# Performance work log

Measured on AMD Instinct MI355X. Metric: run time of the kernel, lower is better.

The kernel has to match this reference:

```python
import jax, jax.numpy as jnp
import numpy as np

IMG_SIZE = 224  # matches init_kwargs img_size


def setup_inputs() -> dict:
    key = jax.random.key(0)
    k1, k2, k3 = jax.random.split(key, 3)
    B, N = 128, 16384
    points = jax.random.uniform(k1, (B, N, 3), dtype=jnp.float32, minval=-1.0, maxval=1.0)
    azimuth = jax.random.uniform(k2, (B,), dtype=jnp.float32, minval=0.0, maxval=2.0 * np.pi)
    elevation = jax.random.uniform(k3, (B,), dtype=jnp.float32, minval=-0.5, maxval=0.5)
    return {"points": points, "azimuth": azimuth, "elevation": elevation}


def _rotation_matrices(azimuth, elevation):
    cა, sა = jnp.cos(azimuth), jnp.sin(azimuth)
    ce, se = jnp.cos(elevation), jnp.sin(elevation)
    z = jnp.zeros_like(cა)
    o = jnp.ones_like(cა)
    # R_az: rotation about y-axis, shape (B,3,3)
    R_az = jnp.stack([
        jnp.stack([cა, z, sა], -1),
        jnp.stack([z, o, z], -1),
        jnp.stack([-sა, z, cა], -1),
    ], axis=-2)
    # R_el: rotation about x-axis
    R_el = jnp.stack([
        jnp.stack([o, z, z], -1),
        jnp.stack([z, ce, -se], -1),
        jnp.stack([z, se, ce], -1),
    ], axis=-2)
    return jnp.einsum('bij,bjk->bik', R_el, R_az)


def reference(points, azimuth, elevation):
    B, N, _ = points.shape
    H = W = IMG_SIZE
    R = _rotation_matrices(azimuth, elevation)                 # (B,3,3)
    rotated = jnp.einsum('bni,bji->bnj', points, R)            # points @ R^T -> (B,N,3)

    points_2d = rotated[..., :2]
    z = rotated[..., 2]
    z_min = jnp.min(z, axis=1, keepdims=True)
    z_max = jnp.max(z, axis=1, keepdims=True)
    feat = 0.3 + 0.7 * (z - z_min) / (z_max - z_min + 1e-6)    # (B,N)

    px = (points_2d[..., 0] + 1.0) * 0.5 * W - 0.5
    py = (points_2d[..., 1] + 1.0) * 0.5 * H - 0.5
    px1 = jnp.floor(px); py1 = jnp.floor(py)
    px2 = px1 + 1.0;     py2 = py1 + 1.0

    w11 = (px2 - px) * (py2 - py)
    w12 = (px2 - px) * (py - py1)
    w21 = (px - px1) * (py2 - py)
    w22 = (px - px1) * (py - py1)

    mask = (px1 >= 0) & (py1 >= 0) & (px2 < W) & (py2 < H)     # (B,N)
    # fuse mask + feature into the weights instead of compacting (jit-friendly)
    vals = jnp.stack([w11, w12, w21, w22], axis=-1)            # (B,N,4)
    vals = vals * (feat * mask.astype(feat.dtype))[..., None]

    px1i = jnp.clip(px1, 0, W - 1).astype(jnp.int32)
    py1i = jnp.clip(py1, 0, H - 1).astype(jnp.int32)
    px2i = jnp.clip(px2, 0, W - 1).astype(jnp.int32)
    py2i = jnp.clip(py2, 0, H - 1).astype(jnp.int32)
    base = (jnp.arange(B, dtype=jnp.int32) * (H * W))[:, None]  # (B,1)
    idx = jnp.stack([
        base + py1i * W + px1i,
        base + py2i * W + px1i,
        base + py1i * W + px2i,
        base + py2i * W + px2i,
    ], axis=-1)                                                 # (B,N,4)

    image = jnp.zeros(B * H * W, dtype=vals.dtype)
    image = image.at[idx.reshape(-1)].add(vals.reshape(-1))
    image = image.reshape(B, 1, H, W)
    return jnp.broadcast_to(image, (B, 3, H, W))
```

## Files before the change

kernel.cpp:

```cpp
#include <hip/hip_runtime.h>

#define IMG 224
#define HW (IMG * IMG)
#define NB 128
#define NPTS 16384

#define QUARTERS 4
#define RPB (IMG / QUARTERS)
#define TILE_FLOATS (RPB * IMG)

#define PARAMS_STRIDE 12

__global__ __launch_bounds__(1024) void k_minmax(const float* __restrict__ pts,
                                                 const float* __restrict__ az,
                                                 const float* __restrict__ el,
                                                 float* __restrict__ params) {
    const int b = blockIdx.x;
    const int tid = threadIdx.x;

    float sa, ca, se, ce;
    __sincosf(az[b], &sa, &ca);
    __sincosf(el[b], &se, &ce);
    const float r20 = -ce * sa, r21 = se, r22 = ce * ca;

    const float* __restrict__ pb = pts + (size_t)b * NPTS * 3;

    float zmin = 1e30f, zmax = -1e30f;
    for (int n = tid; n < NPTS; n += 1024) {
        const float x = pb[n * 3 + 0];
        const float y = pb[n * 3 + 1];
        const float z = pb[n * 3 + 2];
        const float rz = r20 * x + r21 * y + r22 * z;
        zmin = fminf(zmin, rz);
        zmax = fmaxf(zmax, rz);
    }

    __shared__ float smin[1024], smax[1024];
    smin[tid] = zmin;
    smax[tid] = zmax;
    __syncthreads();
    for (int s = 512; s > 0; s >>= 1) {
        if (tid < s) {
            smin[tid] = fminf(smin[tid], smin[tid + s]);
            smax[tid] = fmaxf(smax[tid], smax[tid + s]);
        }
        __syncthreads();
    }

    if (tid == 0) {
        float* P = params + (size_t)b * PARAMS_STRIDE;
        P[0] = ca;       P[1] = 0.f; P[2] = sa;
        P[3] = se * sa;  P[4] = ce;  P[5] = -se * ca;
        P[6] = r20;      P[7] = r21; P[8] = r22;
        P[9] = smin[0];
        P[10] = 0.7f / (smax[0] - smin[0] + 1e-6f);
    }
}

__global__ __launch_bounds__(256) void k_splat(const float* __restrict__ pts,
                                               const float* __restrict__ params,
                                               float* __restrict__ out) {
    const int b = blockIdx.x >> 2;
    const int q = blockIdx.x & 3;
    const int y0 = q * RPB;

    __shared__ float tile[TILE_FLOATS];
    for (int i = threadIdx.x; i < TILE_FLOATS; i += 256) tile[i] = 0.0f;

    const float* __restrict__ P = params + (size_t)b * PARAMS_STRIDE;
    const float r00 = P[0], r02 = P[2];
    const float r10 = P[3], r11 = P[4], r12 = P[5];
    const float r20 = P[6], r21 = P[7], r22 = P[8];
    const float zmin = P[9], inv = P[10];

    const float* __restrict__ pb = pts + (size_t)b * NPTS * 3;
    __syncthreads();

    for (int n = threadIdx.x; n < NPTS; n += 256) {
        const float x = pb[n * 3 + 0];
        const float y = pb[n * 3 + 1];
        const float z = pb[n * 3 + 2];

        const float rx = r00 * x + r02 * z;
        const float ry = r10 * x + r11 * y + r12 * z;
        const float rz = r20 * x + r21 * y + r22 * z;

        const float feat = 0.3f + (rz - zmin) * inv;

        const float px = (rx + 1.0f) * (0.5f * IMG) - 0.5f;
        const float py = (ry + 1.0f) * (0.5f * IMG) - 0.5f;
        const float px1 = floorf(px);
        const float py1 = floorf(py);
        const float px2 = px1 + 1.0f;
        const float py2 = py1 + 1.0f;

        if (px1 >= 0.0f && py1 >= 0.0f && px2 < (float)IMG && py2 < (float)IMG) {
            const float wx2 = px - px1;
            const float wx1 = px2 - px;
            const float wy2 = py - py1;
            const float wy1 = py2 - py;

            const int ix = (int)px1;
            const int iy = (int)py1;
            const int r0 = iy - y0;
            const int r1 = r0 + 1;

            if (r0 >= 0 && r0 < RPB) {
                atomicAdd(&tile[r0 * IMG + ix],     wx1 * wy1 * feat);
                atomicAdd(&tile[r0 * IMG + ix + 1], wx2 * wy1 * feat);
            }
            if (r1 >= 0 && r1 < RPB) {
                atomicAdd(&tile[r1 * IMG + ix],     wx1 * wy2 * feat);
                atomicAdd(&tile[r1 * IMG + ix + 1], wx2 * wy2 * feat);
            }
        }
    }

    __syncthreads();

    const float4* __restrict__ t4 = (const float4*)tile;
    float4* __restrict__ o4 = (float4*)(out + (size_t)b * 3 * HW + (size_t)y0 * IMG);
    const int HW4 = HW / 4;
#pragma unroll
    for (int i = threadIdx.x; i < TILE_FLOATS / 4; i += 256) {
        const float4 v = t4[i];
        o4[i] = v;
        o4[i + HW4] = v;
        o4[i + 2 * HW4] = v;
    }
}

extern "C" void kernel_launch(void* const* d_in, const int* in_sizes, int n_in,
                              void* d_out, int out_size, void* d_ws, size_t ws_size,
                              hipStream_t stream) {
    const float* pts = (const float*)d_in[0];
    const float* az  = (const float*)d_in[1];
    const float* el  = (const float*)d_in[2];
    float* params = (float*)d_ws;
    float* out = (float*)d_out;

    k_minmax<<<NB, 1024, 0, stream>>>(pts, az, el, params);
    k_splat<<<NB * QUARTERS, 256, 0, stream>>>(pts, params, out);
}
```

Measured before the change: 143.8 us.

## Fuse min/max reduction into splat kernel with vectorized point loads

Merges the separate z-range kernel into the splat kernel, so each quarter-tile block computes the per-batch z min/max itself with wave shuffles and a small shared reduction. This drops one launch and the params round trip through global memory. Point loads become float4 triples, each handling four points, and the block size grows to 512 threads. In exchange, every one of the four blocks per batch now rereads the points for the reduction, which is redundant work, though the second pass likely hits in cache.

```diff
diff --git a/kernel.cpp b/kernel.cpp
--- a/kernel.cpp
+++ b/kernel.cpp
@@ -2,109 +2,84 @@
 
 #define IMG 224
 #define HW (IMG * IMG)
+#define HW4 (HW / 4)
 #define NB 128
 #define NPTS 16384
 
 #define QUARTERS 4
 #define RPB (IMG / QUARTERS)
 #define TILE_FLOATS (RPB * IMG)
+#define THREADS 512
 
-#define PARAMS_STRIDE 12
+__global__ __launch_bounds__(THREADS) void k_render(const float* __restrict__ pts,
+                                                    const float* __restrict__ az,
+                                                    const float* __restrict__ el,
+                                                    float* __restrict__ out) {
+    const int b = blockIdx.x & (NB - 1);
+    const int q = blockIdx.x >> 7;
+    const int y0 = q * RPB;
 
-__global__ __launch_bounds__(1024) void k_minmax(const float* __restrict__ pts,
-                                                 const float* __restrict__ az,
-                                                 const float* __restrict__ el,
-                                                 float* __restrict__ params) {
-    const int b = blockIdx.x;
-    const int tid = threadIdx.x;
+    __shared__ float tile[TILE_FLOATS];
+    __shared__ float wmin[THREADS / 64], wmax[THREADS / 64];
 
     float sa, ca, se, ce;
     __sincosf(az[b], &sa, &ca);
     __sincosf(el[b], &se, &ce);
-    const float r20 = -ce * sa, r21 = se, r22 = ce * ca;
+    const float r00 = ca,       r02 = sa;
+    const float r10 = se * sa,  r11 = ce,  r12 = -se * ca;
+    const float r20 = -ce * sa, r21 = se,  r22 = ce * ca;
 
-    const float* __restrict__ pb = pts + (size_t)b * NPTS * 3;
+    for (int i = threadIdx.x; i < TILE_FLOATS; i += THREADS) tile[i] = 0.0f;
+
+    const float4* __restrict__ pb4 = (const float4*)(pts + (size_t)b * NPTS * 3);
 
     float zmin = 1e30f, zmax = -1e30f;
-    for (int n = tid; n < NPTS; n += 1024) {
-        const float x = pb[n * 3 + 0];
-        const float y = pb[n * 3 + 1];
-        const float z = pb[n * 3 + 2];
-        const float rz = r20 * x + r21 * y + r22 * z;
-        zmin = fminf(zmin, rz);
-        zmax = fmaxf(zmax, rz);
+    for (int it = 0; it < NPTS / (4 * THREADS); ++it) {
+        const int t = it * THREADS + threadIdx.x;
+        const float4 v0 = pb4[3 * t + 0];
+        const float4 v1 = pb4[3 * t + 1];
+        const float4 v2 = pb4[3 * t + 2];
+        float rz;
+        rz = r20 * v0.x + r21 * v0.y + r22 * v0.z; zmin = fminf(zmin, rz); zmax = fmaxf(zmax, rz);
+        rz = r20 * v0.w + r21 * v1.x + r22 * v1.y; zmin = fminf(zmin, rz); zmax = fmaxf(zmax, rz);
+        rz = r20 * v1.z + r21 * v1.w + r22 * v2.x; zmin = fminf(zmin, rz); zmax = fmaxf(zmax, rz);
+        rz = r20 * v2.y + r21 * v2.z + r22 * v2.w; zmin = fminf(zmin, rz); zmax = fmaxf(zmax, rz);
     }
+    for (int m = 1; m < 64; m <<= 1) {
+        zmin = fminf(zmin, __shfl_xor(zmin, m));
+        zmax = fmaxf(zmax, __shfl_xor(zmax, m));
+    }
+    const int wid = threadIdx.x >> 6;
+    if ((threadIdx.x & 63) == 0) { wmin[wid] = zmin; wmax[wid] = zmax; }
+    __syncthreads();
+    zmin = wmin[0]; zmax = wmax[0];
+#pragma unroll
+    for (int w = 1; w < THREADS / 64; ++w) {
+        zmin = fminf(zmin, wmin[w]);
+        zmax = fmaxf(zmax, wmax[w]);
+    }
+    const float inv = 0.7f / (zmax - zmin + 1e-6f);
 
-    __shared__ float smin[1024], smax[1024];
-    smin[tid] = zmin;
-    smax[tid] = zmax;
-    __syncthreads();
-    for (int s = 512; s > 0; s >>= 1) {
-        if (tid < s) {
-            smin[tid] = fminf(smin[tid], smin[tid + s]);
-            smax[tid] = fmaxf(smax[tid], smax[tid + s]);
-        }
-        __syncthreads();
-    }
-
-    if (tid == 0) {
-        float* P = params + (size_t)b * PARAMS_STRIDE;
-        P[0] = ca;       P[1] = 0.f; P[2] = sa;
-        P[3] = se * sa;  P[4] = ce;  P[5] = -se * ca;
-        P[6] = r20;      P[7] = r21; P[8] = r22;
-        P[9] = smin[0];
-        P[10] = 0.7f / (smax[0] - smin[0] + 1e-6f);
-    }
-}
-
-__global__ __launch_bounds__(256) void k_splat(const float* __restrict__ pts,
-                                               const float* __restrict__ params,
-                                               float* __restrict__ out) {
-    const int b = blockIdx.x >> 2;
-    const int q = blockIdx.x & 3;
-    const int y0 = q * RPB;
-
-    __shared__ float tile[TILE_FLOATS];
-    for (int i = threadIdx.x; i < TILE_FLOATS; i += 256) tile[i] = 0.0f;
-
-    const float* __restrict__ P = params + (size_t)b * PARAMS_STRIDE;
-    const float r00 = P[0], r02 = P[2];
-    const float r10 = P[3], r11 = P[4], r12 = P[5];
-    const float r20 = P[6], r21 = P[7], r22 = P[8];
-    const float zmin = P[9], inv = P[10];
-
-    const float* __restrict__ pb = pts + (size_t)b * NPTS * 3;
-    __syncthreads();
-
-    for (int n = threadIdx.x; n < NPTS; n += 256) {
-        const float x = pb[n * 3 + 0];
-        const float y = pb[n * 3 + 1];
-        const float z = pb[n * 3 + 2];
-
+    auto splat = [&](float x, float y, float z) {
         const float rx = r00 * x + r02 * z;
         const float ry = r10 * x + r11 * y + r12 * z;
         const float rz = r20 * x + r21 * y + r22 * z;
-
         const float feat = 0.3f + (rz - zmin) * inv;
 
         const float px = (rx + 1.0f) * (0.5f * IMG) - 0.5f;
         const float py = (ry + 1.0f) * (0.5f * IMG) - 0.5f;
         const float px1 = floorf(px);
         const float py1 = floorf(py);
-        const float px2 = px1 + 1.0f;
-        const float py2 = py1 + 1.0f;
-
-        if (px1 >= 0.0f && py1 >= 0.0f && px2 < (float)IMG && py2 < (float)IMG) {
+        if (px1 >= 0.0f && py1 >= 0.0f && px1 < (float)(IMG - 1) && py1 < (float)(IMG - 1)) {
             const float wx2 = px - px1;
-            const float wx1 = px2 - px;
+            const float wx1 = 1.0f - wx2;
             const float wy2 = py - py1;
-            const float wy1 = py2 - py;
+            const float wy1 = 1.0f - wy2;
 
             const int ix = (int)px1;
             const int iy = (int)py1;
             const int r0 = iy - y0;
             const int r1 = r0 + 1;
-
             if (r0 >= 0 && r0 < RPB) {
                 atomicAdd(&tile[r0 * IMG + ix],     wx1 * wy1 * feat);
                 atomicAdd(&tile[r0 * IMG + ix + 1], wx2 * wy1 * feat);
@@ -114,15 +89,24 @@
                 atomicAdd(&tile[r1 * IMG + ix + 1], wx2 * wy2 * feat);
             }
         }
+    };
+
+    for (int it = 0; it < NPTS / (4 * THREADS); ++it) {
+        const int t = it * THREADS + threadIdx.x;
+        const float4 v0 = pb4[3 * t + 0];
+        const float4 v1 = pb4[3 * t + 1];
+        const float4 v2 = pb4[3 * t + 2];
+        splat(v0.x, v0.y, v0.z);
+        splat(v0.w, v1.x, v1.y);
+        splat(v1.z, v1.w, v2.x);
+        splat(v2.y, v2.z, v2.w);
     }
 
     __syncthreads();
 
     const float4* __restrict__ t4 = (const float4*)tile;
     float4* __restrict__ o4 = (float4*)(out + (size_t)b * 3 * HW + (size_t)y0 * IMG);
-    const int HW4 = HW / 4;
-#pragma unroll
-    for (int i = threadIdx.x; i < TILE_FLOATS / 4; i += 256) {
+    for (int i = threadIdx.x; i < TILE_FLOATS / 4; i += THREADS) {
         const float4 v = t4[i];
         o4[i] = v;
         o4[i + HW4] = v;
@@ -136,9 +120,7 @@
     const float* pts = (const float*)d_in[0];
     const float* az  = (const float*)d_in[1];
     const float* el  = (const float*)d_in[2];
-    float* params = (float*)d_ws;
     float* out = (float*)d_out;
 
-    k_minmax<<<NB, 1024, 0, stream>>>(pts, az, el, params);
-    k_splat<<<NB * QUARTERS, 256, 0, stream>>>(pts, params, out);
+    k_render<<<NB * QUARTERS, THREADS, 0, stream>>>(pts, az, el, out);
 }
```

Result: faster. 133.5 us (-7.1%).
